# Kernel optimization log

Hardware: AMD Instinct MI355X
Metric: run time of the kernel (lower is better)

## Reference

```python
import jax, jax.numpy as jnp
import numpy as np

EMBED_DIM = 1024
NUM_HEADS = 16
HEAD_DIM = EMBED_DIM // NUM_HEADS


def setup_inputs() -> dict:
    key = jax.random.key(0)
    k1, k2, k3, k4 = jax.random.split(key, 4)
    B, N, D = 4, 2048, EMBED_DIM
    x = jax.random.normal(k1, (B, N, D), dtype=jnp.float32)
    # torch nn.Linear layout: weight [out_features, in_features]
    w_qkv = jax.random.normal(k2, (3 * D, D), dtype=jnp.float32) * (1.0 / np.sqrt(D))
    w_out = jax.random.normal(k3, (D, D), dtype=jnp.float32) * (1.0 / np.sqrt(D))
    b_out = jax.random.normal(k4, (D,), dtype=jnp.float32) * 0.01
    return {"x": x, "w_qkv": w_qkv, "w_out": w_out, "b_out": b_out}


def reference(x, w_qkv, w_out, b_out):
    B, N, D = x.shape
    H, Hd = NUM_HEADS, HEAD_DIM
    qkv = (x @ w_qkv.T).reshape(B, N, 3, H, Hd)
    q, k, v = qkv[:, :, 0], qkv[:, :, 1], qkv[:, :, 2]  # [B,N,H,Hd]
    # NOTE: contracts over BOTH heads and head_dim -> single shared [B,N,N] map
    scores = jnp.einsum('bnhd,bmhd->bnm', q, k) / np.sqrt(Hd).astype(np.float32)
    attn = jax.nn.softmax(scores, axis=-1)
    out = jnp.einsum('bnm,bmhd->bnhd', attn, v).reshape(B, N, D)
    return out @ w_out.T + b_out
```

## Files before the change

kernel.cpp:

```cpp
#include <hip/hip_runtime.h>


typedef __bf16 bf16;
typedef __attribute__((ext_vector_type(8))) __bf16 bf16x8;
typedef __attribute__((ext_vector_type(4))) __bf16 bf16x4;
typedef __attribute__((ext_vector_type(16))) float f32x16;

#define BATCH 4
#define NTOK  2048
#define DIM   1024
#define MROWS (BATCH * NTOK)
#define QKVC  (3 * DIM)

__device__ __forceinline__ void async16(const bf16* g, bf16* l) {
  __builtin_amdgcn_global_load_lds(
      (const __attribute__((address_space(1))) void*)g,
      (__attribute__((address_space(3))) void*)l, 16, 0, 0);
}

__global__ void f32_to_bf16(const float* __restrict__ in, bf16* __restrict__ out, int n) {
  int i = (blockIdx.x * blockDim.x + threadIdx.x) * 4;
  if (i < n) {
    float4 f = *(const float4*)(in + i);
    bf16x4 o;
    o.x = (bf16)f.x; o.y = (bf16)f.y; o.z = (bf16)f.z; o.w = (bf16)f.w;
    *(bf16x4*)(out + i) = o;
  }
}

__global__ void zero_f32(float* __restrict__ p, int n) {
  int i = blockIdx.x * blockDim.x + threadIdx.x;
  if (i < n) p[i] = 0.f;
}

struct GemmCore {
  const bf16 *ga0, *ga1, *gb0, *gb1;
  int sIdx0, sIdx1;
  int wm, wn, l31, half;
};

__device__ __forceinline__ GemmCore gemm_setup(const bf16* A, const bf16* Bm,
                                               int lda, int ldb,
                                               long rowA, long rowB) {
  GemmCore g;
  const int tid = threadIdx.x;
  const int wave = tid >> 6, lane = tid & 63;
  g.wm = (wave >> 1) << 6;
  g.wn = (wave & 1) << 6;
  g.l31 = lane & 31;
  g.half = lane >> 5;
  const int srow = tid >> 2;
  const int sc   = tid & 3;
  const int scol = (sc ^ (srow & 3)) << 3;
  g.ga0 = A  + (rowA + srow)      * (long)lda + scol;
  g.ga1 = A  + (rowA + srow + 64) * (long)lda + scol;
  g.gb0 = Bm + (rowB + srow)      * (long)ldb + scol;
  g.gb1 = Bm + (rowB + srow + 64) * (long)ldb + scol;
  g.sIdx0 = srow * 32 + sc * 8;
  g.sIdx1 = (srow + 64) * 32 + sc * 8;
  return g;
}

__device__ __forceinline__ void gemm_kloop(const GemmCore& g, int K,
                                           bf16* As, bf16* Bs, f32x16 acc[2][2]) {
  const int sw = g.l31 & 3;
  for (int kt = 0; kt < K; kt += 32) {
    async16(g.ga0 + kt, As + g.sIdx0);
    async16(g.ga1 + kt, As + g.sIdx1);
    async16(g.gb0 + kt, Bs + g.sIdx0);
    async16(g.gb1 + kt, Bs + g.sIdx1);
    __syncthreads();

    bf16x8 af[2][2], bfm[2][2];
#pragma unroll
    for (int ti = 0; ti < 2; ++ti)
#pragma unroll
      for (int s = 0; s < 2; ++s)
        af[ti][s] = *(const bf16x8*)&As[(g.wm + ti * 32 + g.l31) * 32 + ((s * 2 + g.half) ^ sw) * 8];
#pragma unroll
    for (int tj = 0; tj < 2; ++tj)
#pragma unroll
      for (int s = 0; s < 2; ++s)
        bfm[tj][s] = *(const bf16x8*)&Bs[(g.wn + tj * 32 + g.l31) * 32 + ((s * 2 + g.half) ^ sw) * 8];

#pragma unroll
    for (int s = 0; s < 2; ++s)
#pragma unroll
      for (int ti = 0; ti < 2; ++ti)
#pragma unroll
        for (int tj = 0; tj < 2; ++tj)
          acc[ti][tj] = __builtin_amdgcn_mfma_f32_32x32x16_bf16(
              af[ti][s], bfm[tj][s], acc[ti][tj], 0, 0, 0);

    __syncthreads();
  }
}

template <int MODE>
__launch_bounds__(256)
__global__ void gemm_bt(const bf16* __restrict__ Aroot, const bf16* __restrict__ Broot,
                        void* __restrict__ Croot, const float* __restrict__ bias,
                        const float* __restrict__ Lroot,
                        int K, int lda, int ldb, int ldc,
                        long strideA, long strideB, long strideC) {
  const bf16* A  = Aroot + (long)blockIdx.z * strideA;
  const bf16* Bm = Broot + (long)blockIdx.z * strideB;
  __shared__ alignas(16) bf16 As[128 * 32];
  __shared__ alignas(16) bf16 Bs[128 * 32];

  const long rowA = (long)blockIdx.y * 128;
  const long rowB = (long)blockIdx.x * 128;
  GemmCore g = gemm_setup(A, Bm, lda, ldb, rowA, rowB);

  f32x16 acc[2][2] = {};
  gemm_kloop(g, K, As, Bs, acc);

  if constexpr (MODE == 0) {
    bf16* C = (bf16*)Croot + (long)blockIdx.z * strideC;
#pragma unroll
    for (int ti = 0; ti < 2; ++ti)
#pragma unroll
      for (int tj = 0; tj < 2; ++tj) {
        const long col = rowB + g.wn + tj * 32 + g.l31;
#pragma unroll
        for (int r = 0; r < 16; ++r) {
          const long row = rowA + g.wm + ti * 32 + (r & 3) + 8 * (r >> 2) + 4 * g.half;
          C[row * (long)ldc + col] = (bf16)acc[ti][tj][r];
        }
      }
  } else {
    float* C = (float*)Croot + (long)blockIdx.z * strideC;
    const float* L = Lroot + (long)blockIdx.z * NTOK;
#pragma unroll
    for (int ti = 0; ti < 2; ++ti) {
#pragma unroll
      for (int r = 0; r < 16; ++r) {
        const long row = rowA + g.wm + ti * 32 + (r & 3) + 8 * (r >> 2) + 4 * g.half;
        const float inv = 1.0f / L[row];
#pragma unroll
        for (int tj = 0; tj < 2; ++tj) {
          const long col = rowB + g.wn + tj * 32 + g.l31;
          C[row * (long)ldc + col] = acc[ti][tj][r] * inv + bias[col];
        }
      }
    }
  }
}

__launch_bounds__(256)
__global__ void gemm_sv(const bf16* __restrict__ QKV, const bf16* __restrict__ Wout,
                        bf16* __restrict__ E, bf16* __restrict__ Vpp,
                        float* __restrict__ Lroot) {
  __shared__ alignas(16) bf16 As[128 * 32];
  __shared__ alignas(16) bf16 Bs[128 * 32];

  const int z = blockIdx.z;
  if (z < 4) {
    const bf16* A  = QKV + (long)z * NTOK * QKVC;
    const bf16* Bm = A + DIM;
    const long rowA = (long)blockIdx.y * 128;
    const long rowB = (long)blockIdx.x * 128;
    GemmCore g = gemm_setup(A, Bm, QKVC, QKVC, rowA, rowB);
    f32x16 acc[2][2] = {};
    gemm_kloop(g, DIM, As, Bs, acc);

    bf16* C = E + (long)z * NTOK * NTOK;
    float* L = Lroot + (long)z * NTOK;
#pragma unroll
    for (int ti = 0; ti < 2; ++ti) {
#pragma unroll
      for (int r = 0; r < 16; ++r) {
        const long row = rowA + g.wm + ti * 32 + (r & 3) + 8 * (r >> 2) + 4 * g.half;
        float psum = 0.f;
#pragma unroll
        for (int tj = 0; tj < 2; ++tj) {
          const long col = rowB + g.wn + tj * 32 + g.l31;
          float e = __expf(acc[ti][tj][r] * 0.125f);
          bf16 eb = (bf16)e;
          C[row * (long)NTOK + col] = eb;
          psum += (float)eb;
        }
#pragma unroll
        for (int off = 16; off >= 1; off >>= 1) psum += __shfl_xor(psum, off, 64);
        if (g.l31 == 0) atomicAdd(&L[row], psum);
      }
    }
  } else {
    if (blockIdx.y >= 8) return;
    const int b = z - 4;
    const bf16* Bm = QKV + (long)b * NTOK * QKVC + 2 * DIM;
    const long rowA = (long)blockIdx.y * 128;
    const long rowB = (long)blockIdx.x * 128;
    GemmCore g = gemm_setup(Wout, Bm, DIM, QKVC, rowA, rowB);
    f32x16 acc[2][2] = {};
    gemm_kloop(g, DIM, As, Bs, acc);

    bf16* C = Vpp + (long)b * DIM * NTOK;
#pragma unroll
    for (int ti = 0; ti < 2; ++ti)
#pragma unroll
      for (int tj = 0; tj < 2; ++tj) {
        const long col = rowB + g.wn + tj * 32 + g.l31;
#pragma unroll
        for (int r = 0; r < 16; ++r) {
          const long row = rowA + g.wm + ti * 32 + (r & 3) + 8 * (r >> 2) + 4 * g.half;
          C[row * (long)NTOK + col] = (bf16)acc[ti][tj][r];
        }
      }
  }
}

extern "C" void kernel_launch(void* const* d_in, const int* in_sizes, int n_in,
                              void* d_out, int out_size, void* d_ws, size_t ws_size,
                              hipStream_t stream) {
  const float* x      = (const float*)d_in[0];
  const float* w_qkv  = (const float*)d_in[1];
  const float* w_out  = (const float*)d_in[2];
  const float* b_out  = (const float*)d_in[3];
  float* out = (float*)d_out;

  char* w = (char*)d_ws;
  bf16*  Xbf   = (bf16*)(w);
  bf16*  Wqkvb = (bf16*)(w + 16777216);
  bf16*  Woutb = (bf16*)(w + 23068672);
  bf16*  QKV   = (bf16*)(w + 25165824);
  bf16*  E     = (bf16*)(w + 75497472);
  bf16*  Vpp   = (bf16*)(w + 109051904);
  float* L     = (float*)(w + 125829120);

  f32_to_bf16<<<(MROWS * DIM / 4 + 255) / 256, 256, 0, stream>>>(x, Xbf, MROWS * DIM);
  f32_to_bf16<<<(QKVC * DIM / 4 + 255) / 256, 256, 0, stream>>>(w_qkv, Wqkvb, QKVC * DIM);
  f32_to_bf16<<<(DIM * DIM / 4 + 255) / 256, 256, 0, stream>>>(w_out, Woutb, DIM * DIM);
  zero_f32<<<(BATCH * NTOK + 255) / 256, 256, 0, stream>>>(L, BATCH * NTOK);

  gemm_bt<0><<<dim3(QKVC / 128, MROWS / 128, 1), 256, 0, stream>>>(
      Xbf, Wqkvb, QKV, nullptr, nullptr, DIM, DIM, DIM, QKVC, 0, 0, 0);

  gemm_sv<<<dim3(NTOK / 128, NTOK / 128, 2 * BATCH), 256, 0, stream>>>(
      QKV, Woutb, E, Vpp, L);

  gemm_bt<2><<<dim3(DIM / 128, NTOK / 128, BATCH), 256, 0, stream>>>(
      E, Vpp, out, b_out, L, NTOK, NTOK, NTOK, DIM,
      (long)NTOK * NTOK, (long)DIM * NTOK, (long)NTOK * DIM);
}
```

Before: 306.8 us.

## Double GEMM K-tile to 64 and fuse conversion kernels into one prep launch

The shared GEMM K-loop now stages 64-wide K slices instead of 32 in LDS, with an 8-way XOR swizzle and four async loads per operand per thread. This halves the number of barrier pairs per GEMM and gives more MFMA work per synchronisation. The three f32-to-bf16 conversions and the L zeroing are merged into a single launch to cut launch overhead. LDS use per block doubles to 32 KB, which may reduce occupancy, and there is still no double buffering.

```diff
diff --git a/kernel.cpp b/kernel.cpp
--- a/kernel.cpp
+++ b/kernel.cpp
@@ -18,24 +18,32 @@
       (__attribute__((address_space(3))) void*)l, 16, 0, 0);
 }
 
-__global__ void f32_to_bf16(const float* __restrict__ in, bf16* __restrict__ out, int n) {
-  int i = (blockIdx.x * blockDim.x + threadIdx.x) * 4;
-  if (i < n) {
-    float4 f = *(const float4*)(in + i);
-    bf16x4 o;
-    o.x = (bf16)f.x; o.y = (bf16)f.y; o.z = (bf16)f.z; o.w = (bf16)f.w;
-    *(bf16x4*)(out + i) = o;
-  }
-}
-
-__global__ void zero_f32(float* __restrict__ p, int n) {
+__device__ __forceinline__ void cvt4(const float* in, bf16* out, int i4) {
+  float4 f = *(const float4*)(in + i4 * 4);
+  bf16x4 o;
+  o.x = (bf16)f.x; o.y = (bf16)f.y; o.z = (bf16)f.z; o.w = (bf16)f.w;
+  *(bf16x4*)(out + i4 * 4) = o;
+}
+
+__global__ void prep(const float* __restrict__ x, const float* __restrict__ wqkv,
+                     const float* __restrict__ wout,
+                     bf16* __restrict__ Xbf, bf16* __restrict__ Wqkvb,
+                     bf16* __restrict__ Woutb, float* __restrict__ L) {
+  const int nx = MROWS * DIM / 4, nq = QKVC * DIM / 4, nw = DIM * DIM / 4;
+  const int nl = BATCH * NTOK / 4;
   int i = blockIdx.x * blockDim.x + threadIdx.x;
-  if (i < n) p[i] = 0.f;
+  if (i < nx) cvt4(x, Xbf, i);
+  else if (i < nx + nq) cvt4(wqkv, Wqkvb, i - nx);
+  else if (i < nx + nq + nw) cvt4(wout, Woutb, i - nx - nq);
+  else if (i < nx + nq + nw + nl) {
+    float4 z = {0.f, 0.f, 0.f, 0.f};
+    *(float4*)(L + (i - nx - nq - nw) * 4) = z;
+  }
 }
 
 struct GemmCore {
-  const bf16 *ga0, *ga1, *gb0, *gb1;
-  int sIdx0, sIdx1;
+  const bf16 *ga[4], *gb[4];
+  int sIdx[4];
   int wm, wn, l31, half;
 };
 
@@ -49,42 +57,43 @@
   g.wn = (wave & 1) << 6;
   g.l31 = lane & 31;
   g.half = lane >> 5;
-  const int srow = tid >> 2;
-  const int sc   = tid & 3;
-  const int scol = (sc ^ (srow & 3)) << 3;
-  g.ga0 = A  + (rowA + srow)      * (long)lda + scol;
-  g.ga1 = A  + (rowA + srow + 64) * (long)lda + scol;
-  g.gb0 = Bm + (rowB + srow)      * (long)ldb + scol;
-  g.gb1 = Bm + (rowB + srow + 64) * (long)ldb + scol;
-  g.sIdx0 = srow * 32 + sc * 8;
-  g.sIdx1 = (srow + 64) * 32 + sc * 8;
+  const int srow = tid >> 3;
+  const int sc   = tid & 7;
+  const int scol = (sc ^ (srow & 7)) << 3;
+#pragma unroll
+  for (int seg = 0; seg < 4; ++seg) {
+    g.ga[seg] = A  + (rowA + srow + 32 * seg) * (long)lda + scol;
+    g.gb[seg] = Bm + (rowB + srow + 32 * seg) * (long)ldb + scol;
+    g.sIdx[seg] = (srow + 32 * seg) * 64 + sc * 8;
+  }
   return g;
 }
 
 __device__ __forceinline__ void gemm_kloop(const GemmCore& g, int K,
                                            bf16* As, bf16* Bs, f32x16 acc[2][2]) {
-  const int sw = g.l31 & 3;
-  for (int kt = 0; kt < K; kt += 32) {
-    async16(g.ga0 + kt, As + g.sIdx0);
-    async16(g.ga1 + kt, As + g.sIdx1);
-    async16(g.gb0 + kt, Bs + g.sIdx0);
-    async16(g.gb1 + kt, Bs + g.sIdx1);
+  const int sw = g.l31 & 7;
+  for (int kt = 0; kt < K; kt += 64) {
+#pragma unroll
+    for (int seg = 0; seg < 4; ++seg) {
+      async16(g.ga[seg] + kt, As + g.sIdx[seg]);
+      async16(g.gb[seg] + kt, Bs + g.sIdx[seg]);
+    }
     __syncthreads();
 
-    bf16x8 af[2][2], bfm[2][2];
+    bf16x8 af[2][4], bfm[2][4];
 #pragma unroll
     for (int ti = 0; ti < 2; ++ti)
 #pragma unroll
-      for (int s = 0; s < 2; ++s)
-        af[ti][s] = *(const bf16x8*)&As[(g.wm + ti * 32 + g.l31) * 32 + ((s * 2 + g.half) ^ sw) * 8];
+      for (int s = 0; s < 4; ++s)
+        af[ti][s] = *(const bf16x8*)&As[(g.wm + ti * 32 + g.l31) * 64 + ((s * 2 + g.half) ^ sw) * 8];
 #pragma unroll
     for (int tj = 0; tj < 2; ++tj)
 #pragma unroll
-      for (int s = 0; s < 2; ++s)
-        bfm[tj][s] = *(const bf16x8*)&Bs[(g.wn + tj * 32 + g.l31) * 32 + ((s * 2 + g.half) ^ sw) * 8];
-
-#pragma unroll
-    for (int s = 0; s < 2; ++s)
+      for (int s = 0; s < 4; ++s)
+        bfm[tj][s] = *(const bf16x8*)&Bs[(g.wn + tj * 32 + g.l31) * 64 + ((s * 2 + g.half) ^ sw) * 8];
+
+#pragma unroll
+    for (int s = 0; s < 4; ++s)
 #pragma unroll
       for (int ti = 0; ti < 2; ++ti)
 #pragma unroll
@@ -105,8 +114,8 @@
                         long strideA, long strideB, long strideC) {
   const bf16* A  = Aroot + (long)blockIdx.z * strideA;
   const bf16* Bm = Broot + (long)blockIdx.z * strideB;
-  __shared__ alignas(16) bf16 As[128 * 32];
-  __shared__ alignas(16) bf16 Bs[128 * 32];
+  __shared__ alignas(16) bf16 As[128 * 64];
+  __shared__ alignas(16) bf16 Bs[128 * 64];
 
   const long rowA = (long)blockIdx.y * 128;
   const long rowB = (long)blockIdx.x * 128;
@@ -151,8 +160,8 @@
 __global__ void gemm_sv(const bf16* __restrict__ QKV, const bf16* __restrict__ Wout,
                         bf16* __restrict__ E, bf16* __restrict__ Vpp,
                         float* __restrict__ Lroot) {
-  __shared__ alignas(16) bf16 As[128 * 32];
-  __shared__ alignas(16) bf16 Bs[128 * 32];
+  __shared__ alignas(16) bf16 As[128 * 64];
+  __shared__ alignas(16) bf16 Bs[128 * 64];
 
   const int z = blockIdx.z;
   if (z < 4) {
@@ -228,10 +237,10 @@
   bf16*  Vpp   = (bf16*)(w + 109051904);
   float* L     = (float*)(w + 125829120);
 
-  f32_to_bf16<<<(MROWS * DIM / 4 + 255) / 256, 256, 0, stream>>>(x, Xbf, MROWS * DIM);
-  f32_to_bf16<<<(QKVC * DIM / 4 + 255) / 256, 256, 0, stream>>>(w_qkv, Wqkvb, QKVC * DIM);
-  f32_to_bf16<<<(DIM * DIM / 4 + 255) / 256, 256, 0, stream>>>(w_out, Woutb, DIM * DIM);
-  zero_f32<<<(BATCH * NTOK + 255) / 256, 256, 0, stream>>>(L, BATCH * NTOK);
+  {
+    const int n4 = MROWS * DIM / 4 + QKVC * DIM / 4 + DIM * DIM / 4 + BATCH * NTOK / 4;
+    prep<<<(n4 + 255) / 256, 256, 0, stream>>>(x, w_qkv, w_out, Xbf, Wqkvb, Woutb, L);
+  }
 
   gemm_bt<0><<<dim3(QKVC / 128, MROWS / 128, 1), 256, 0, stream>>>(
       Xbf, Wqkvb, QKV, nullptr, nullptr, DIM, DIM, DIM, QKVC, 0, 0, 0);
```

Measured after the change: 267.9 us. -12.7%, faster.
